# Kernel tuning notes

Hardware: AMD Instinct MI355X
Metric: run time of the kernel (lower is better)

## Reference

```python
import jax, jax.numpy as jnp
import numpy as np

B = 65536
D = 1024
EPS = 1e-5


def setup_inputs() -> dict:
    key = jax.random.key(0)
    ks = jax.random.split(key, 24)
    s = 0.02
    inp = {
        "local_features": jax.random.normal(ks[0], (B, D), jnp.float32),
        "tactical_features": jax.random.normal(ks[1], (B, D), jnp.float32),
        "strategic_features": jax.random.normal(ks[2], (B, D), jnp.float32),
    }
    i = 3
    for name in ["l2t", "t2s", "s2t", "t2l"]:
        inp[f"{name}_w_in"] = jax.random.normal(ks[i], (3 * D, D), jnp.float32) * s; i += 1
        inp[f"{name}_b_in"] = jax.random.normal(ks[i], (3 * D,), jnp.float32) * s; i += 1
        inp[f"{name}_w_out"] = jax.random.normal(ks[i], (D, D), jnp.float32) * s; i += 1
        inp[f"{name}_b_out"] = jax.random.normal(ks[i], (D,), jnp.float32) * s; i += 1
    for j in (1, 2, 3):
        inp[f"ln{j}_g"] = jnp.ones((D,), jnp.float32)
        inp[f"ln{j}_b"] = jnp.zeros((D,), jnp.float32)
    return inp


def _ln(x, g, b):
    m = jnp.mean(x, axis=-1, keepdims=True)
    v = jnp.mean((x - m) ** 2, axis=-1, keepdims=True)
    return (x - m) / jnp.sqrt(v + EPS) * g + b


def _mha_seq1(q_in, kv_in, w_in, b_in, w_out, b_out):
    # nn.MultiheadAttention with seq_len=1: softmax over a single key == 1
    # (and has zero gradient wrt the score), so the attention output equals
    # the value projection of kv; q/k projections drop out of the math.
    d = q_in.shape[-1]
    wv = w_in[2 * d:]
    bv = b_in[2 * d:]
    v = kv_in @ wv.T + bv          # [B, D]
    return v @ w_out.T + b_out      # [B, D]


def reference(local_features, tactical_features, strategic_features,
              l2t_w_in, l2t_b_in, l2t_w_out, l2t_b_out,
              t2s_w_in, t2s_b_in, t2s_w_out, t2s_b_out,
              s2t_w_in, s2t_b_in, s2t_w_out, s2t_b_out,
              t2l_w_in, t2l_b_in, t2l_w_out, t2l_b_out,
              ln1_g, ln1_b, ln2_g, ln2_b, ln3_g, ln3_b):
    tac_upd = _mha_seq1(tactical_features, local_features, l2t_w_in, l2t_b_in, l2t_w_out, l2t_b_out)
    tac = _ln(tactical_features + tac_upd, ln1_g, ln1_b)
    strat_upd = _mha_seq1(strategic_features, tac, t2s_w_in, t2s_b_in, t2s_w_out, t2s_b_out)
    strat = _ln(strategic_features + strat_upd, ln2_g, ln2_b)
    tac_guide = _mha_seq1(tac, strat, s2t_w_in, s2t_b_in, s2t_w_out, s2t_b_out)
    tac = _ln(tac + tac_guide, ln3_g, ln3_b)
    loc_guide = _mha_seq1(local_features, tac, t2l_w_in, t2l_b_in, t2l_w_out, t2l_b_out)
    loc = local_features + loc_guide
    return (loc, tac, strat)
```

## Files before the change

### kernel.cpp

```cpp
#include <hip/hip_runtime.h>

#define D_DIM 1024
#define B_ROWS 65536
#define NKT 16
#define TILE_U16 8192

typedef unsigned short u16;
typedef __attribute__((ext_vector_type(8))) __bf16 bf16x8;
typedef __attribute__((ext_vector_type(4))) float f32x4;
typedef __attribute__((ext_vector_type(8))) unsigned short u16x8;

typedef const __attribute__((address_space(1))) void* gas_cptr;
typedef __attribute__((address_space(3))) void* las_ptr;

__device__ __forceinline__ u16 f2bf(float f) {
  union { float fv; unsigned int i; } v; v.fv = f;
  return (u16)((v.i + 0x7FFFu + ((v.i >> 16) & 1u)) >> 16);
}
__device__ __forceinline__ float bf2f(u16 u) {
  union { unsigned int i; float f; } v; v.i = ((unsigned int)u) << 16; return v.f;
}


template <int RESID, int OUTM>
__global__ __launch_bounds__(256, 4) void gemm_pk(
    const u16* __restrict__ Ap, const u16* __restrict__ Wp,
    const float* __restrict__ bias, const float* __restrict__ Rf, void* Op)
{
  __shared__ __align__(16) u16 smem[2 * TILE_U16];
  u16* sA = smem;
  u16* sB = smem + TILE_U16;

  const int bm = blockIdx.y, bn = blockIdx.x;
  const int tid = threadIdx.x;
  const int wave = tid >> 6;
  const int lane = tid & 63;
  const int wm = wave >> 1, wn = wave & 1;
  const int fr = lane & 15;
  const int l4 = lane >> 4;

  const u16* Abase = Ap + (size_t)bm * NKT * TILE_U16;
  const u16* Wbase = Wp + (size_t)bn * NKT * TILE_U16;

  f32x4 acc[4][4] = {};

  for (int kt = 0; kt < NKT; ++kt) {
    const u16* at = Abase + kt * TILE_U16;
    const u16* wt = Wbase + kt * TILE_U16;
#pragma unroll
    for (int i = 0; i < 4; ++i) {
      __builtin_amdgcn_global_load_lds((gas_cptr)(at + (i * 256 + tid) * 8),
                                       (las_ptr)(sA + (i * 256 + tid) * 8), 16, 0, 0);
      __builtin_amdgcn_global_load_lds((gas_cptr)(wt + (i * 256 + tid) * 8),
                                       (las_ptr)(sB + (i * 256 + tid) * 8), 16, 0, 0);
    }
    __syncthreads();
#pragma unroll
    for (int ks = 0; ks < 2; ++ks) {
      bf16x8 af[4], bf[4];
#pragma unroll
      for (int m = 0; m < 4; ++m) {
        const int row = wm * 64 + m * 16 + fr;
        af[m] = *(const bf16x8*)&sA[row * 64 + (((ks * 4 + l4) ^ (row & 7)) * 8)];
      }
#pragma unroll
      for (int n = 0; n < 4; ++n) {
        const int row = wn * 64 + n * 16 + fr;
        bf[n] = *(const bf16x8*)&sB[row * 64 + (((ks * 4 + l4) ^ (row & 7)) * 8)];
      }
#pragma unroll
      for (int m = 0; m < 4; ++m)
#pragma unroll
        for (int n = 0; n < 4; ++n)
          acc[m][n] = __builtin_amdgcn_mfma_f32_16x16x32_bf16(af[m], bf[n], acc[m][n], 0, 0, 0);
    }
    __syncthreads();
  }

  float* eC = (float*)smem;
  const int q4 = l4 * 4;
#pragma unroll
  for (int H = 0; H < 2; ++H) {
    if (wm == H) {
#pragma unroll
      for (int m = 0; m < 4; ++m)
#pragma unroll
        for (int j = 0; j < 4; ++j) {
          const int r = m * 16 + q4 + j;
#pragma unroll
          for (int n = 0; n < 4; ++n) {
            const int c = wn * 64 + n * 16 + fr;
            const int c4 = c >> 2;
            eC[r * 128 + ((c4 ^ ((r >> 2) & 7)) * 4) + (c & 3)] = acc[m][n][j];
          }
        }
    }
    __syncthreads();
#pragma unroll
    for (int it = 0; it < 4; ++it) {
      const int idx = it * 256 + tid;
      const int r = idx >> 4;
      const int g8 = idx & 15;
      const int gr = bm * 128 + H * 64 + r;
      const int c4a = g8 * 2, c4b = g8 * 2 + 1;
      const int rx = (r >> 2) & 7;
      f32x4 c0 = *(const f32x4*)&eC[r * 128 + ((c4a ^ rx) * 4)];
      f32x4 c1 = *(const f32x4*)&eC[r * 128 + ((c4b ^ rx) * 4)];
      const int gc0 = bn * 128 + g8 * 8;
      if (bias) {
        f32x4 b0 = *(const f32x4*)&bias[gc0];
        f32x4 b1 = *(const f32x4*)&bias[gc0 + 4];
#pragma unroll
        for (int t = 0; t < 4; ++t) { c0[t] += b0[t]; c1[t] += b1[t]; }
      }
      if (RESID == 1) {
        const float* rp = Rf + (size_t)gr * D_DIM + gc0;
        f32x4 r0 = *(const f32x4*)rp;
        f32x4 r1 = *(const f32x4*)(rp + 4);
#pragma unroll
        for (int t = 0; t < 4; ++t) { c0[t] += r0[t]; c1[t] += r1[t]; }
      }
      if (OUTM == 1) {
        float* op = (float*)Op + (size_t)gr * D_DIM + gc0;
        *(f32x4*)op = c0;
        *(f32x4*)(op + 4) = c1;
      } else {
        const int t_r = gr >> 7, rr = gr & 127;
        const int kt = gc0 >> 6, gs = (gc0 & 63) >> 3;
        const size_t P = ((size_t)(t_r * NKT + kt) * 128 + rr) * 64 + ((gs ^ (rr & 7)) * 8);
        u16x8 ov;
#pragma unroll
        for (int t = 0; t < 4; ++t) { ov[t] = f2bf(c0[t]); ov[t + 4] = f2bf(c1[t]); }
        *(u16x8*)&((u16*)Op)[P] = ov;
      }
    }
    __syncthreads();
  }
}

template <int OF32, int OPK>
__global__ __launch_bounds__(256, 2) void ln_pk(
    const u16* __restrict__ Yp, const float* __restrict__ Rf,
    const float* __restrict__ lng, const float* __restrict__ lnb,
    float* __restrict__ of32, u16* __restrict__ opk)
{
  const int tile = blockIdx.x;
  const int gidx = blockIdx.y * 256 + threadIdx.x;
  const int r = gidx >> 3;
  const int g = gidx & 7;
  const int gc = g ^ (r & 7);
  const size_t grow = (size_t)tile * 128 + r;

  float z[16][8];
  float s = 0.f, ss = 0.f;
#pragma unroll
  for (int kt = 0; kt < 16; ++kt) {
    u16x8 v = *(const u16x8*)&Yp[((size_t)(tile * NKT + kt) * 128) * 64 + (size_t)gidx * 8];
    const float* rp = Rf + grow * D_DIM + kt * 64 + gc * 8;
    f32x4 r0 = *(const f32x4*)rp;
    f32x4 r1 = *(const f32x4*)(rp + 4);
#pragma unroll
    for (int e = 0; e < 4; ++e) {
      z[kt][e] = bf2f(v[e]) + r0[e];
      z[kt][e + 4] = bf2f(v[e + 4]) + r1[e];
    }
#pragma unroll
    for (int e = 0; e < 8; ++e) { s += z[kt][e]; ss += z[kt][e] * z[kt][e]; }
  }
  s += __shfl_xor(s, 1, 64);  ss += __shfl_xor(ss, 1, 64);
  s += __shfl_xor(s, 2, 64);  ss += __shfl_xor(ss, 2, 64);
  s += __shfl_xor(s, 4, 64);  ss += __shfl_xor(ss, 4, 64);
  const float mean = s * (1.f / 1024.f);
  const float var = ss * (1.f / 1024.f) - mean * mean;
  const float rstd = rsqrtf(var + 1e-5f);

#pragma unroll
  for (int kt = 0; kt < 16; ++kt) {
    f32x4 g0 = *(const f32x4*)&lng[kt * 64 + gc * 8];
    f32x4 g1 = *(const f32x4*)&lng[kt * 64 + gc * 8 + 4];
    f32x4 b0 = *(const f32x4*)&lnb[kt * 64 + gc * 8];
    f32x4 b1 = *(const f32x4*)&lnb[kt * 64 + gc * 8 + 4];
    f32x4 o0, o1;
#pragma unroll
    for (int e = 0; e < 4; ++e) {
      o0[e] = (z[kt][e] - mean) * rstd * g0[e] + b0[e];
      o1[e] = (z[kt][e + 4] - mean) * rstd * g1[e] + b1[e];
    }
    if (OPK) {
      u16x8 ov;
#pragma unroll
      for (int e = 0; e < 4; ++e) { ov[e] = f2bf(o0[e]); ov[e + 4] = f2bf(o1[e]); }
      *(u16x8*)&opk[((size_t)(tile * NKT + kt) * 128) * 64 + (size_t)gidx * 8] = ov;
    }
    if (OF32) {
      float* op = of32 + grow * D_DIM + kt * 64 + gc * 8;
      *(f32x4*)op = o0;
      *(f32x4*)(op + 4) = o1;
    }
  }
}

__global__ __launch_bounds__(256) void pack_pk(const float* __restrict__ src,
                                               u16* __restrict__ dst)
{
  const int t_r = blockIdx.x;
#pragma unroll 4
  for (int i = 0; i < 64; ++i) {
    const int idx = i * 256 + threadIdx.x;
    const int r = idx >> 7;
    const int gsf = idx & 127;
    const float* sp = src + (size_t)(t_r * 128 + r) * D_DIM + gsf * 8;
    f32x4 a = *(const f32x4*)sp;
    f32x4 b = *(const f32x4*)(sp + 4);
    u16x8 o;
#pragma unroll
    for (int t = 0; t < 4; ++t) { o[t] = f2bf(a[t]); o[t + 4] = f2bf(b[t]); }
    const int kt = gsf >> 3, g3 = gsf & 7;
    *(u16x8*)&dst[((size_t)(t_r * NKT + kt) * 128 + r) * 64 + ((g3 ^ (r & 7)) * 8)] = o;
  }
}

struct TP4 { const float* s[4]; u16* d[4]; };

__global__ __launch_bounds__(256) void transpose_pack(TP4 p) {
  __shared__ float tile[32][33];
  const int z = blockIdx.z;
  const float* src = p.s[z];
  u16* dst = p.d[z];
  const int tx = threadIdx.x & 31, ty = threadIdx.x >> 5;
  const int gx = blockIdx.x * 32, gy = blockIdx.y * 32;
#pragma unroll
  for (int i = 0; i < 4; ++i) {
    const int r = ty + i * 8;
    tile[r][tx] = src[(size_t)(gy + r) * D_DIM + gx + tx];
  }
  __syncthreads();
#pragma unroll
  for (int i = 0; i < 4; ++i) {
    const int drow = gx + ty + i * 8;
    const int dcol = gy + tx;
    const int t_n = drow >> 7, rr = drow & 127;
    const int kt = dcol >> 6, gs = (dcol >> 3) & 7, e = dcol & 7;
    dst[((size_t)(t_n * NKT + kt) * 128 + rr) * 64 + ((gs ^ (rr & 7)) * 8) + e] =
        f2bf(tile[tx][ty + i * 8]);
  }
}

struct BiasArgs { const float* wout[4]; const float* bin[4]; const float* bout[4]; };

__global__ __launch_bounds__(256) void bias_kernel(BiasArgs p, float* cb) {
  const int z = blockIdx.z;
  const int i = blockIdx.x * 256 + threadIdx.x;
  const float* wrow = p.wout[z] + (size_t)i * D_DIM;
  const float* bv = p.bin[z] + 2 * D_DIM;
  float s = 0.f;
  for (int j = 0; j < D_DIM; j += 4) {
    f32x4 w4 = *(const f32x4*)&wrow[j];
    f32x4 b4 = *(const f32x4*)&bv[j];
#pragma unroll
    for (int t = 0; t < 4; ++t) s += w4[t] * b4[t];
  }
  cb[(size_t)z * D_DIM + i] = s + p.bout[z][i];
}

extern "C" void kernel_launch(void* const* d_in, const int* in_sizes, int n_in,
                              void* d_out, int out_size, void* d_ws, size_t ws_size,
                              hipStream_t stream) {
  (void)in_sizes; (void)n_in; (void)out_size; (void)ws_size;
  const size_t BD = (size_t)B_ROWS * D_DIM;
  const size_t DD = (size_t)D_DIM * D_DIM;

  const float* feat_local = (const float*)d_in[0];
  const float* feat_tact  = (const float*)d_in[1];
  const float* feat_strat = (const float*)d_in[2];
  const float* w_in[4]  = {(const float*)d_in[3],  (const float*)d_in[7],  (const float*)d_in[11], (const float*)d_in[15]};
  const float* b_in[4]  = {(const float*)d_in[4],  (const float*)d_in[8],  (const float*)d_in[12], (const float*)d_in[16]};
  const float* w_out[4] = {(const float*)d_in[5],  (const float*)d_in[9],  (const float*)d_in[13], (const float*)d_in[17]};
  const float* b_out[4] = {(const float*)d_in[6],  (const float*)d_in[10], (const float*)d_in[14], (const float*)d_in[18]};
  const float* ln_g[3] = {(const float*)d_in[19], (const float*)d_in[21], (const float*)d_in[23]};
  const float* ln_b[3] = {(const float*)d_in[20], (const float*)d_in[22], (const float*)d_in[24]};

  u16* pkA = (u16*)d_ws;
  u16* pkY = pkA + BD;
  u16* pkB = pkY + BD;
  float* tacF = (float*)(pkB + BD);
  u16* wvT  = (u16*)(tacF + BD);
  u16* wobf = wvT + 4 * DD;
  u16* Wc   = wobf + 4 * DD;
  float* cb = (float*)(Wc + 4 * DD);

  float* out = (float*)d_out;
  float* o_loc = out;
  float* o_tac = out + BD;
  float* o_str = out + 2 * BD;

  hipLaunchKernelGGL(pack_pk, dim3(512), dim3(256), 0, stream, feat_local, pkA);
  for (int z = 0; z < 4; ++z)
    hipLaunchKernelGGL(pack_pk, dim3(8), dim3(256), 0, stream, w_out[z], wobf + z * DD);

  TP4 tp;
  for (int z = 0; z < 4; ++z) { tp.s[z] = w_in[z] + 2 * DD; tp.d[z] = wvT + z * DD; }
  hipLaunchKernelGGL(transpose_pack, dim3(32, 32, 4), dim3(256), 0, stream, tp);

  BiasArgs ba;
  for (int z = 0; z < 4; ++z) { ba.wout[z] = w_out[z]; ba.bin[z] = b_in[z]; ba.bout[z] = b_out[z]; }
  hipLaunchKernelGGL(bias_kernel, dim3(4, 1, 4), dim3(256), 0, stream, ba, cb);

  for (int z = 0; z < 4; ++z)
    hipLaunchKernelGGL((gemm_pk<0, 2>), dim3(8, 8), dim3(256), 0, stream,
                       wobf + z * DD, wvT + z * DD, (const float*)nullptr,
                       (const float*)nullptr, (void*)(Wc + z * DD));

  hipLaunchKernelGGL((gemm_pk<0, 2>), dim3(8, 512), dim3(256), 0, stream,
                     pkA, Wc + 0 * DD, cb + 0, (const float*)nullptr, (void*)pkY);
  hipLaunchKernelGGL((ln_pk<1, 1>), dim3(512, 4), dim3(256), 0, stream,
                     pkY, feat_tact, ln_g[0], ln_b[0], tacF, pkB);

  hipLaunchKernelGGL((gemm_pk<0, 2>), dim3(8, 512), dim3(256), 0, stream,
                     pkB, Wc + 1 * DD, cb + 1024, (const float*)nullptr, (void*)pkY);
  hipLaunchKernelGGL((ln_pk<1, 1>), dim3(512, 4), dim3(256), 0, stream,
                     pkY, feat_strat, ln_g[1], ln_b[1], o_str, pkA);

  hipLaunchKernelGGL((gemm_pk<0, 2>), dim3(8, 512), dim3(256), 0, stream,
                     pkA, Wc + 2 * DD, cb + 2048, (const float*)nullptr, (void*)pkY);
  hipLaunchKernelGGL((ln_pk<1, 1>), dim3(512, 4), dim3(256), 0, stream,
                     pkY, tacF, ln_g[2], ln_b[2], o_tac, pkB);

  hipLaunchKernelGGL((gemm_pk<1, 1>), dim3(8, 512), dim3(256), 0, stream,
                     pkB, Wc + 3 * DD, cb + 3072, feat_local, (void*)o_loc);
}
```

Baseline: 1.482 ms.

## Fuse residual adds into GEMM epilogues and batch weight-prep launches

New measurement: 1.327 ms. 1.12x faster.

```diff
diff --git a/kernel.cpp b/kernel.cpp
--- a/kernel.cpp
+++ b/kernel.cpp
@@ -25,12 +25,13 @@
 template <int RESID, int OUTM>
 __global__ __launch_bounds__(256, 4) void gemm_pk(
     const u16* __restrict__ Ap, const u16* __restrict__ Wp,
-    const float* __restrict__ bias, const float* __restrict__ Rf, void* Op)
+    const float* __restrict__ bias, const void* Rp, void* Op, size_t zs)
 {
   __shared__ __align__(16) u16 smem[2 * TILE_U16];
   u16* sA = smem;
   u16* sB = smem + TILE_U16;
 
+  const size_t zoff = (size_t)blockIdx.z * zs;
   const int bm = blockIdx.y, bn = blockIdx.x;
   const int tid = threadIdx.x;
   const int wave = tid >> 6;
@@ -39,8 +40,8 @@
   const int fr = lane & 15;
   const int l4 = lane >> 4;
 
-  const u16* Abase = Ap + (size_t)bm * NKT * TILE_U16;
-  const u16* Wbase = Wp + (size_t)bn * NKT * TILE_U16;
+  const u16* Abase = Ap + zoff + (size_t)bm * NKT * TILE_U16;
+  const u16* Wbase = Wp + zoff + (size_t)bn * NKT * TILE_U16;
 
   f32x4 acc[4][4] = {};
 
@@ -78,6 +79,8 @@
   }
 
   float* eC = (float*)smem;
+  const float* Rf = (const float*)Rp;
+  const u16*   Rb = (const u16*)Rp;
   const int q4 = l4 * 4;
 #pragma unroll
   for (int H = 0; H < 2; ++H) {
@@ -120,6 +123,14 @@
 #pragma unroll
         for (int t = 0; t < 4; ++t) { c0[t] += r0[t]; c1[t] += r1[t]; }
       }
+      if (RESID == 2) {
+        const int t_r = gr >> 7, rr = gr & 127;
+        const int kt = gc0 >> 6, gs = (gc0 & 63) >> 3;
+        const size_t P = ((size_t)(t_r * NKT + kt) * 128 + rr) * 64 + ((gs ^ (rr & 7)) * 8);
+        u16x8 rv = *(const u16x8*)&Rb[P];
+#pragma unroll
+        for (int t = 0; t < 4; ++t) { c0[t] += bf2f(rv[t]); c1[t] += bf2f(rv[t + 4]); }
+      }
       if (OUTM == 1) {
         float* op = (float*)Op + (size_t)gr * D_DIM + gc0;
         *(f32x4*)op = c0;
@@ -131,7 +142,7 @@
         u16x8 ov;
 #pragma unroll
         for (int t = 0; t < 4; ++t) { ov[t] = f2bf(c0[t]); ov[t + 4] = f2bf(c1[t]); }
-        *(u16x8*)&((u16*)Op)[P] = ov;
+        *(u16x8*)&((u16*)Op + zoff)[P] = ov;
       }
     }
     __syncthreads();
@@ -140,7 +151,7 @@
 
 template <int OF32, int OPK>
 __global__ __launch_bounds__(256, 2) void ln_pk(
-    const u16* __restrict__ Yp, const float* __restrict__ Rf,
+    const u16* __restrict__ Yp,
     const float* __restrict__ lng, const float* __restrict__ lnb,
     float* __restrict__ of32, u16* __restrict__ opk)
 {
@@ -156,16 +167,11 @@
 #pragma unroll
   for (int kt = 0; kt < 16; ++kt) {
     u16x8 v = *(const u16x8*)&Yp[((size_t)(tile * NKT + kt) * 128) * 64 + (size_t)gidx * 8];
-    const float* rp = Rf + grow * D_DIM + kt * 64 + gc * 8;
-    f32x4 r0 = *(const f32x4*)rp;
-    f32x4 r1 = *(const f32x4*)(rp + 4);
-#pragma unroll
-    for (int e = 0; e < 4; ++e) {
-      z[kt][e] = bf2f(v[e]) + r0[e];
-      z[kt][e + 4] = bf2f(v[e + 4]) + r1[e];
-    }
-#pragma unroll
-    for (int e = 0; e < 8; ++e) { s += z[kt][e]; ss += z[kt][e] * z[kt][e]; }
+#pragma unroll
+    for (int e = 0; e < 8; ++e) {
+      z[kt][e] = bf2f(v[e]);
+      s += z[kt][e]; ss += z[kt][e] * z[kt][e];
+    }
   }
   s += __shfl_xor(s, 1, 64);  ss += __shfl_xor(ss, 1, 64);
   s += __shfl_xor(s, 2, 64);  ss += __shfl_xor(ss, 2, 64);
@@ -220,6 +226,29 @@
   }
 }
 
+struct PW4 { const float* s[4]; u16* d[4]; };
+
+__global__ __launch_bounds__(256) void pack_w4(PW4 p) {
+  const int t_r = blockIdx.x;
+  const int z = blockIdx.y;
+  const float* src = p.s[z];
+  u16* dst = p.d[z];
+#pragma unroll 4
+  for (int i = 0; i < 64; ++i) {
+    const int idx = i * 256 + threadIdx.x;
+    const int r = idx >> 7;
+    const int gsf = idx & 127;
+    const float* sp = src + (size_t)(t_r * 128 + r) * D_DIM + gsf * 8;
+    f32x4 a = *(const f32x4*)sp;
+    f32x4 b = *(const f32x4*)(sp + 4);
+    u16x8 o;
+#pragma unroll
+    for (int t = 0; t < 4; ++t) { o[t] = f2bf(a[t]); o[t + 4] = f2bf(b[t]); }
+    const int kt = gsf >> 3, g3 = gsf & 7;
+    *(u16x8*)&dst[((size_t)(t_r * NKT + kt) * 128 + r) * 64 + ((g3 ^ (r & 7)) * 8)] = o;
+  }
+}
+
 struct TP4 { const float* s[4]; u16* d[4]; };
 
 __global__ __launch_bounds__(256) void transpose_pack(TP4 p) {
@@ -283,8 +312,7 @@
   u16* pkA = (u16*)d_ws;
   u16* pkY = pkA + BD;
   u16* pkB = pkY + BD;
-  float* tacF = (float*)(pkB + BD);
-  u16* wvT  = (u16*)(tacF + BD);
+  u16* wvT  = pkB + BD;
   u16* wobf = wvT + 4 * DD;
   u16* Wc   = wobf + 4 * DD;
   float* cb = (float*)(Wc + 4 * DD);
@@ -295,8 +323,9 @@
   float* o_str = out + 2 * BD;
 
   hipLaunchKernelGGL(pack_pk, dim3(512), dim3(256), 0, stream, feat_local, pkA);
-  for (int z = 0; z < 4; ++z)
-    hipLaunchKernelGGL(pack_pk, dim3(8), dim3(256), 0, stream, w_out[z], wobf + z * DD);
+  PW4 pw;
+  for (int z = 0; z < 4; ++z) { pw.s[z] = w_out[z]; pw.d[z] = wobf + z * DD; }
+  hipLaunchKernelGGL(pack_w4, dim3(8, 4), dim3(256), 0, stream, pw);
 
   TP4 tp;
   for (int z = 0; z < 4; ++z) { tp.s[z] = w_in[z] + 2 * DD; tp.d[z] = wvT + z * DD; }
@@ -306,26 +335,25 @@
   for (int z = 0; z < 4; ++z) { ba.wout[z] = w_out[z]; ba.bin[z] = b_in[z]; ba.bout[z] = b_out[z]; }
   hipLaunchKernelGGL(bias_kernel, dim3(4, 1, 4), dim3(256), 0, stream, ba, cb);
 
-  for (int z = 0; z < 4; ++z)
-    hipLaunchKernelGGL((gemm_pk<0, 2>), dim3(8, 8), dim3(256), 0, stream,
-                       wobf + z * DD, wvT + z * DD, (const float*)nullptr,
-                       (const float*)nullptr, (void*)(Wc + z * DD));
-
-  hipLaunchKernelGGL((gemm_pk<0, 2>), dim3(8, 512), dim3(256), 0, stream,
-                     pkA, Wc + 0 * DD, cb + 0, (const float*)nullptr, (void*)pkY);
+  hipLaunchKernelGGL((gemm_pk<0, 2>), dim3(8, 8, 4), dim3(256), 0, stream,
+                     wobf, wvT, (const float*)nullptr, (const void*)nullptr,
+                     (void*)Wc, DD);
+
+  hipLaunchKernelGGL((gemm_pk<1, 2>), dim3(8, 512, 1), dim3(256), 0, stream,
+                     pkA, Wc + 0 * DD, cb + 0, (const void*)feat_tact, (void*)pkY, 0);
+  hipLaunchKernelGGL((ln_pk<0, 1>), dim3(512, 4), dim3(256), 0, stream,
+                     pkY, ln_g[0], ln_b[0], (float*)nullptr, pkB);
+
+  hipLaunchKernelGGL((gemm_pk<1, 2>), dim3(8, 512, 1), dim3(256), 0, stream,
+                     pkB, Wc + 1 * DD, cb + 1024, (const void*)feat_strat, (void*)pkY, 0);
   hipLaunchKernelGGL((ln_pk<1, 1>), dim3(512, 4), dim3(256), 0, stream,
-                     pkY, feat_tact, ln_g[0], ln_b[0], tacF, pkB);
-
-  hipLaunchKernelGGL((gemm_pk<0, 2>), dim3(8, 512), dim3(256), 0, stream,
-                     pkB, Wc + 1 * DD, cb + 1024, (const float*)nullptr, (void*)pkY);
+                     pkY, ln_g[1], ln_b[1], o_str, pkA);
+
+  hipLaunchKernelGGL((gemm_pk<2, 2>), dim3(8, 512, 1), dim3(256), 0, stream,
+                     pkA, Wc + 2 * DD, cb + 2048, (const void*)pkB, (void*)pkY, 0);
   hipLaunchKernelGGL((ln_pk<1, 1>), dim3(512, 4), dim3(256), 0, stream,
-                     pkY, feat_strat, ln_g[1], ln_b[1], o_str, pkA);
-
-  hipLaunchKernelGGL((gemm_pk<0, 2>), dim3(8, 512), dim3(256), 0, stream,
-                     pkA, Wc + 2 * DD, cb + 2048, (const float*)nullptr, (void*)pkY);
-  hipLaunchKernelGGL((ln_pk<1, 1>), dim3(512, 4), dim3(256), 0, stream,
-                     pkY, tacF, ln_g[2], ln_b[2], o_tac, pkB);
-
-  hipLaunchKernelGGL((gemm_pk<1, 1>), dim3(8, 512), dim3(256), 0, stream,
-                     pkB, Wc + 3 * DD, cb + 3072, feat_local, (void*)o_loc);
-}
+                     pkY, ln_g[2], ln_b[2], o_tac, pkB);
+
+  hipLaunchKernelGGL((gemm_pk<1, 1>), dim3(8, 512, 1), dim3(256), 0, stream,
+                     pkB, Wc + 3 * DD, cb + 3072, (const void*)feat_local, (void*)o_loc, 0);
+}
```
